# Kernel optimization log

Measured on AMD Instinct MI355X. Metric: run time of the kernel, lower is better.

The kernel has to match this reference:

```python
import jax, jax.numpy as jnp
import numpy as np

N = 1024
C_LOCAL = 384
C_PAIR = 128
HEADS = 8
KEY_SIZE = 32
LN_EPS = 1e-5


def setup_inputs() -> dict:
    key = jax.random.key(0)
    ks = jax.random.split(key, 5)
    local = jax.random.normal(ks[0], (N, C_LOCAL), dtype=jnp.float32)
    pair = jax.random.normal(ks[1], (N, N, C_PAIR), dtype=jnp.float32)
    mask = jnp.ones((N,), dtype=bool)
    ln_scale = jnp.ones((C_LOCAL,), dtype=jnp.float32)
    ln_offset = jnp.zeros((C_LOCAL,), dtype=jnp.float32)
    W_value = jax.random.normal(ks[2], (C_LOCAL, HEADS * KEY_SIZE), dtype=jnp.float32) * (1.0 / np.sqrt(C_LOCAL))
    W_attn = jax.random.normal(ks[3], (C_PAIR, HEADS), dtype=jnp.float32) * (1.0 / np.sqrt(C_PAIR))
    W_out = jax.random.normal(ks[4], (HEADS * KEY_SIZE, C_LOCAL), dtype=jnp.float32) * (1.0 / np.sqrt(HEADS * KEY_SIZE))
    return {"local": local, "pair": pair, "mask": mask,
            "ln_scale": ln_scale, "ln_offset": ln_offset,
            "W_value": W_value, "W_attn": W_attn, "W_out": W_out}


def reference(local, pair, mask, ln_scale, ln_offset, W_value, W_attn, W_out):
    # pair_mask[i, j] = mask[i] & mask[j]
    pair_mask = (mask[:, None] & mask[None, :])[..., None]  # [N, N, 1]

    # LayerNorm over last axis (create_scale=True, create_offset=True)
    mu = jnp.mean(local, axis=-1, keepdims=True)
    var = jnp.var(local, axis=-1, keepdims=True)
    local_ln = (local - mu) * jax.lax.rsqrt(var + LN_EPS) * ln_scale + ln_offset

    # value projection -> [N, heads, key_size]
    value = (local_ln @ W_value).reshape(local.shape[0], HEADS, KEY_SIZE)

    # pair-bias attention logits -> [N, N, heads]
    attn = pair @ W_attn
    attn = jnp.where(pair_mask, attn, -1e9)
    attn = jax.nn.softmax(attn, axis=1)
    attn = jnp.where(pair_mask, attn, 0.0)

    # weighted average over j, per head -> [N, heads, key_size] -> [N, heads*key_size]
    out = jnp.einsum('ijh,jhc->ihc', attn, value).reshape(local.shape[0], -1)
    return out @ W_out
```

## Files before the change

kernel.cpp:

```cpp
#include <hip/hip_runtime.h>
#include <cstddef>

#define NN 1024
#define CL 384
#define CP 128
#define NH 8
#define KS 32
#define HK 256

typedef float floatx4 __attribute__((ext_vector_type(4)));

template<int CTRL>
__device__ __forceinline__ float dpp_mov(float v) {
    return __int_as_float(__builtin_amdgcn_update_dpp(
        0, __float_as_int(v), CTRL, 0xF, 0xF, true));
}

__device__ __forceinline__ float4 ntload4(const float* p) {
    floatx4 t = __builtin_nontemporal_load((const floatx4*)p);
    float4 r; r.x = t.x; r.y = t.y; r.z = t.z; r.w = t.w;
    return r;
}

__global__ __launch_bounds__(256) void k_ln_value(
    const float* __restrict__ local_, const float* __restrict__ ln_scale,
    const float* __restrict__ ln_offset, const float* __restrict__ Wv,
    float* __restrict__ value)
{
    __shared__ float ln_s[4][CL];
    const int tid = threadIdx.x;
    const int w = tid >> 6, lane = tid & 63;
    const int r = blockIdx.x * 4 + w;
    const float* lp = local_ + (size_t)r * CL;
    float x[6]; float s1 = 0.f, s2 = 0.f;
#pragma unroll
    for (int k = 0; k < 6; ++k) { x[k] = lp[lane + 64*k]; s1 += x[k]; s2 += x[k]*x[k]; }
#pragma unroll
    for (int m = 1; m < 64; m <<= 1) { s1 += __shfl_xor(s1, m); s2 += __shfl_xor(s2, m); }
    const float mean = s1 * (1.f/CL);
    const float var  = fmaxf(s2 * (1.f/CL) - mean*mean, 0.f);
    const float rstd = rsqrtf(var + 1e-5f);
#pragma unroll
    for (int k = 0; k < 6; ++k) {
        const int c = lane + 64*k;
        ln_s[w][c] = (x[k]-mean)*rstd*ln_scale[c] + ln_offset[c];
    }
    __syncthreads();
    const int m_ = tid;
    float acc0=0.f, acc1=0.f, acc2=0.f, acc3=0.f;
    for (int c0 = 0; c0 < CL; c0 += 8) {
        float wv[8];
#pragma unroll
        for (int cc = 0; cc < 8; ++cc) wv[cc] = Wv[(size_t)(c0+cc)*HK + m_];
        {
            const float4 a = *(const float4*)&ln_s[0][c0];
            const float4 b = *(const float4*)&ln_s[0][c0+4];
            acc0 += a.x*wv[0]+a.y*wv[1]+a.z*wv[2]+a.w*wv[3]+b.x*wv[4]+b.y*wv[5]+b.z*wv[6]+b.w*wv[7];
        }
        {
            const float4 a = *(const float4*)&ln_s[1][c0];
            const float4 b = *(const float4*)&ln_s[1][c0+4];
            acc1 += a.x*wv[0]+a.y*wv[1]+a.z*wv[2]+a.w*wv[3]+b.x*wv[4]+b.y*wv[5]+b.z*wv[6]+b.w*wv[7];
        }
        {
            const float4 a = *(const float4*)&ln_s[2][c0];
            const float4 b = *(const float4*)&ln_s[2][c0+4];
            acc2 += a.x*wv[0]+a.y*wv[1]+a.z*wv[2]+a.w*wv[3]+b.x*wv[4]+b.y*wv[5]+b.z*wv[6]+b.w*wv[7];
        }
        {
            const float4 a = *(const float4*)&ln_s[3][c0];
            const float4 b = *(const float4*)&ln_s[3][c0+4];
            acc3 += a.x*wv[0]+a.y*wv[1]+a.z*wv[2]+a.w*wv[3]+b.x*wv[4]+b.y*wv[5]+b.z*wv[6]+b.w*wv[7];
        }
    }
    const int rb = blockIdx.x*4;
    value[(size_t)(rb+0)*HK + m_] = acc0;
    value[(size_t)(rb+1)*HK + m_] = acc1;
    value[(size_t)(rb+2)*HK + m_] = acc2;
    value[(size_t)(rb+3)*HK + m_] = acc3;
}

__global__ __launch_bounds__(256, 4) void k_attn(
    const float* __restrict__ pair, const int* __restrict__ mask,
    const float* __restrict__ Wa, const float* __restrict__ value,
    const float* __restrict__ Wo, float* __restrict__ outp)
{
    __shared__ float zf[NN];
    __shared__ float ps[2][NH][68];
    __shared__ float sep[8*NH];
    __shared__ float ov4[4][64][4];
    __shared__ float ov[HK];

    const int tid = threadIdx.x;
    const int g = tid >> 5;
    const int sub5 = tid & 31;
    const int i = blockIdx.x;
    const bool bmi = mask[i] != 0;

    for (int k = tid; k < NN; k += 256)
        zf[k] = (bmi && (mask[k] != 0)) ? 1.f : 0.f;

    float wreg[32];
    {
        const float4* wp = (const float4*)(Wa + sub5*4*NH);
#pragma unroll
        for (int k = 0; k < 8; ++k) {
            const float4 t4 = wp[k];
            wreg[4*k+0]=t4.x; wreg[4*k+1]=t4.y; wreg[4*k+2]=t4.z; wreg[4*k+3]=t4.w;
        }
    }

    const int  myh   = (sub5 & 1)*4 + ((sub5 >> 1) & 1)*2 + ((sub5 >> 3) & 1);
    const bool owner = (sub5 & 0x14) == 0;

    const int q  = tid >> 6;
    const int mq = tid & 63;
    const int pvh = mq >> 3;
    float4 ac4; ac4.x = ac4.y = ac4.z = ac4.w = 0.f;
    float se_loc = 0.f;

    const float* pb = pair + (size_t)i*NN*CP + sub5*4;

    float4 d[8];
#pragma unroll
    for (int s = 0; s < 8; ++s)
        d[s] = ntload4(pb + (size_t)(g*8 + s)*CP);

    __syncthreads();

    for (int ci = 0; ci < 16; ++ci) {
        const int b = ci & 1;
        const int jc = ci * 64;

#pragma unroll
        for (int s = 0; s < 8; ++s) {
            const float4 cur = d[s];
            float acc[8];
#pragma unroll
            for (int h = 0; h < 8; ++h)
                acc[h] = cur.x*wreg[h] + cur.y*wreg[8+h] + cur.z*wreg[16+h] + cur.w*wreg[24+h];
            const bool b0 = (sub5 & 1) != 0;
            const bool b1 = (sub5 & 2) != 0;
            const bool b3 = (sub5 & 8) != 0;
            float r4[4];
#pragma unroll
            for (int k = 0; k < 4; ++k)
                r4[k] = (b0 ? acc[k+4] : acc[k]) + dpp_mov<0xB1>(b0 ? acc[k] : acc[k+4]);
            float r2[2];
#pragma unroll
            for (int k = 0; k < 2; ++k)
                r2[k] = (b1 ? r4[k+2] : r4[k]) + dpp_mov<0x4E>(b1 ? r4[k] : r4[k+2]);
            float r1 = (b3 ? r2[1] : r2[0]) + dpp_mov<0x128>(b3 ? r2[0] : r2[1]);
            r1 += __shfl_xor(r1, 4);
            r1 += __shfl_xor(r1, 16);
            const int jj = g*8 + s;
            const float pt = zf[jc + jj] * __expf(r1);
            se_loc += pt;
            ps[b][myh][jj] = pt;
        }

        if (ci != 15) {
            const int jb = jc + 64 + g*8;
#pragma unroll
            for (int s = 0; s < 8; ++s)
                d[s] = ntload4(pb + (size_t)(jb + s)*CP);
        }

        if (ci > 0) {
            const int pbuf = (ci - 1) & 1;
            const float* vb = value + (size_t)(jc - 64)*HK + mq*4;
#pragma unroll 4
            for (int k = 0; k < 16; ++k) {
                const int jj = 4*k + q;
                const float p = ps[pbuf][pvh][jj];
                const float4 v4 = *(const float4*)(vb + (size_t)jj*HK);
                ac4.x += p*v4.x; ac4.y += p*v4.y; ac4.z += p*v4.z; ac4.w += p*v4.w;
            }
        }

        asm volatile("s_waitcnt lgkmcnt(0)" ::: "memory");
        __builtin_amdgcn_s_barrier();
    }

    {
        const float* vb = value + (size_t)(15*64)*HK + mq*4;
#pragma unroll 4
        for (int k = 0; k < 16; ++k) {
            const int jj = 4*k + q;
            const float p = ps[1][pvh][jj];
            const float4 v4 = *(const float4*)(vb + (size_t)jj*HK);
            ac4.x += p*v4.x; ac4.y += p*v4.y; ac4.z += p*v4.z; ac4.w += p*v4.w;
        }
    }

    if (owner) sep[g*NH + myh] = se_loc;
    ov4[q][mq][0] = ac4.x; ov4[q][mq][1] = ac4.y;
    ov4[q][mq][2] = ac4.z; ov4[q][mq][3] = ac4.w;
    __syncthreads();

    {
        const int m = tid;
        const float s4 = ov4[0][m>>2][m&3] + ov4[1][m>>2][m&3]
                       + ov4[2][m>>2][m&3] + ov4[3][m>>2][m&3];
        const int h = m >> 5;
        float se = 0.f;
#pragma unroll
        for (int k = 0; k < 8; ++k) se += sep[k*NH + h];
        const float inv = (se > 0.f) ? (1.f/se) : 0.f;
        ov[m] = s4 * inv;
    }
    __syncthreads();

    for (int o = tid; o < CL; o += 256) {
        float a0 = 0.f;
        for (int m = 0; m < HK; m += 4) {
            const float4 x0 = *(const float4*)&ov[m];
            a0 += x0.x*Wo[(size_t)(m+0)*CL + o] + x0.y*Wo[(size_t)(m+1)*CL + o]
                + x0.z*Wo[(size_t)(m+2)*CL + o] + x0.w*Wo[(size_t)(m+3)*CL + o];
        }
        outp[(size_t)i*CL + o] = a0;
    }
}

extern "C" void kernel_launch(void* const* d_in, const int* in_sizes, int n_in,
                              void* d_out, int out_size, void* d_ws, size_t ws_size,
                              hipStream_t stream)
{
    (void)in_sizes; (void)n_in; (void)out_size; (void)ws_size;
    const float* local_ = (const float*)d_in[0];
    const float* pair   = (const float*)d_in[1];
    const int*   mask   = (const int*)d_in[2];
    const float* scale  = (const float*)d_in[3];
    const float* offset = (const float*)d_in[4];
    const float* Wv     = (const float*)d_in[5];
    const float* Wa     = (const float*)d_in[6];
    const float* Wo     = (const float*)d_in[7];
    float* value = (float*)d_ws;
    k_ln_value<<<NN/4, 256, 0, stream>>>(local_, scale, offset, Wv, value);
    k_attn<<<NN, 256, 0, stream>>>(pair, mask, Wa, value, Wo, (float*)d_out);
}
```

Before: 149.0 us.

## Restructure attention loop into 32-row chunks with two-deep register prefetch

The pair-logit loop now works on 32-row chunks and keeps two register buffers (dA/dB) of pair data in flight. Each buffer is refilled two chunks ahead, and scheduling barriers keep the prefetch loads from being reordered. The aim is to keep more HBM loads outstanding and hide streaming latency behind the logit and PV compute. The cost is twice as many block barriers, with the same register footprint for the pair data.

```diff
diff --git a/kernel.cpp b/kernel.cpp
--- a/kernel.cpp
+++ b/kernel.cpp
@@ -7,6 +7,8 @@
 #define NH 8
 #define KS 32
 #define HK 256
+#define CHK 32
+#define NCHK (NN/CHK)
 
 typedef float floatx4 __attribute__((ext_vector_type(4)));
 
@@ -86,7 +88,7 @@
     const float* __restrict__ Wo, float* __restrict__ outp)
 {
     __shared__ float zf[NN];
-    __shared__ float ps[2][NH][68];
+    __shared__ float ps[2][NH][CHK+4];
     __shared__ float sep[8*NH];
     __shared__ float ov4[4][64][4];
     __shared__ float ov[HK];
@@ -121,19 +123,17 @@
 
     const float* pb = pair + (size_t)i*NN*CP + sub5*4;
 
-    float4 d[8];
-#pragma unroll
-    for (int s = 0; s < 8; ++s)
-        d[s] = ntload4(pb + (size_t)(g*8 + s)*CP);
-
-    __syncthreads();
-
-    for (int ci = 0; ci < 16; ++ci) {
-        const int b = ci & 1;
-        const int jc = ci * 64;
-
-#pragma unroll
-        for (int s = 0; s < 8; ++s) {
+    float4 dA[4], dB[4];
+
+    auto PREFETCH = [&](float4* d, int jc) {
+#pragma unroll
+        for (int s = 0; s < 4; ++s)
+            d[s] = ntload4(pb + (size_t)(jc + g*4 + s)*CP);
+    };
+
+    auto LOGITS = [&](const float4* d, int jc, int pbuf) {
+#pragma unroll
+        for (int s = 0; s < 4; ++s) {
             const float4 cur = d[s];
             float acc[8];
 #pragma unroll
@@ -153,45 +153,44 @@
             float r1 = (b3 ? r2[1] : r2[0]) + dpp_mov<0x128>(b3 ? r2[0] : r2[1]);
             r1 += __shfl_xor(r1, 4);
             r1 += __shfl_xor(r1, 16);
-            const int jj = g*8 + s;
+            const int jj = g*4 + s;
             const float pt = zf[jc + jj] * __expf(r1);
             se_loc += pt;
-            ps[b][myh][jj] = pt;
-        }
-
-        if (ci != 15) {
-            const int jb = jc + 64 + g*8;
-#pragma unroll
-            for (int s = 0; s < 8; ++s)
-                d[s] = ntload4(pb + (size_t)(jb + s)*CP);
-        }
-
-        if (ci > 0) {
-            const int pbuf = (ci - 1) & 1;
-            const float* vb = value + (size_t)(jc - 64)*HK + mq*4;
-#pragma unroll 4
-            for (int k = 0; k < 16; ++k) {
-                const int jj = 4*k + q;
-                const float p = ps[pbuf][pvh][jj];
-                const float4 v4 = *(const float4*)(vb + (size_t)jj*HK);
-                ac4.x += p*v4.x; ac4.y += p*v4.y; ac4.z += p*v4.z; ac4.w += p*v4.w;
-            }
-        }
-
+            ps[pbuf][myh][jj] = pt;
+        }
+    };
+
+    auto PV = [&](int jc, int pbuf) {
+        const float* vb = value + (size_t)jc*HK + mq*4;
+#pragma unroll
+        for (int k = 0; k < 8; ++k) {
+            const int jj = 4*k + q;
+            const float p = ps[pbuf][pvh][jj];
+            const float4 v4 = *(const float4*)(vb + (size_t)jj*HK);
+            ac4.x += p*v4.x; ac4.y += p*v4.y; ac4.z += p*v4.z; ac4.w += p*v4.w;
+        }
+    };
+
+    PREFETCH(dA, 0);
+    PREFETCH(dB, CHK);
+    __syncthreads();
+
+    for (int it = 0; it < NCHK/2; ++it) {
+        const int k0 = it*2;
+        LOGITS(dA, k0*CHK, 0);
+        if (k0 > 0) PV((k0-1)*CHK, 1);
+        __builtin_amdgcn_sched_barrier(0);
+        if (k0+2 < NCHK) PREFETCH(dA, (k0+2)*CHK);
         asm volatile("s_waitcnt lgkmcnt(0)" ::: "memory");
         __builtin_amdgcn_s_barrier();
-    }
-
-    {
-        const float* vb = value + (size_t)(15*64)*HK + mq*4;
-#pragma unroll 4
-        for (int k = 0; k < 16; ++k) {
-            const int jj = 4*k + q;
-            const float p = ps[1][pvh][jj];
-            const float4 v4 = *(const float4*)(vb + (size_t)jj*HK);
-            ac4.x += p*v4.x; ac4.y += p*v4.y; ac4.z += p*v4.z; ac4.w += p*v4.w;
-        }
-    }
+        LOGITS(dB, (k0+1)*CHK, 1);
+        PV(k0*CHK, 0);
+        __builtin_amdgcn_sched_barrier(0);
+        if (k0+3 < NCHK) PREFETCH(dB, (k0+3)*CHK);
+        asm volatile("s_waitcnt lgkmcnt(0)" ::: "memory");
+        __builtin_amdgcn_s_barrier();
+    }
+    PV((NCHK-1)*CHK, 1);
 
     if (owner) sep[g*NH + myh] = se_loc;
     ov4[q][mq][0] = ac4.x; ov4[q][mq][1] = ac4.y;
```

Measured after the change: 164.5 us. +10.4%, slower.

## Stream pair and value tiles into LDS via async global_load_lds double buffering

Applied to the files above, without the earlier changes.

Replaces the register-held nontemporal prefetch of the pair row with direct global-to-LDS async loads (global_load_lds). The pair row is now processed in 16-row double-buffered tiles, and value rows are staged into LDS per tile as well, with vmcnt waits doing the synchronisation. The aim is to relieve register pressure and overlap memory traffic with compute. In exchange it uses smaller chunks with two barriers per chunk, which means many more iterations and barriers, and occupancy drops to 2 blocks via launch bounds plus a much larger LDS footprint.

```diff
diff --git a/kernel.cpp b/kernel.cpp
--- a/kernel.cpp
+++ b/kernel.cpp
@@ -7,8 +7,8 @@
 #define NH 8
 #define KS 32
 #define HK 256
-
-typedef float floatx4 __attribute__((ext_vector_type(4)));
+#define CKR 16
+#define NB (NN/CKR)
 
 template<int CTRL>
 __device__ __forceinline__ float dpp_mov(float v) {
@@ -16,10 +16,10 @@
         0, __float_as_int(v), CTRL, 0xF, 0xF, true));
 }
 
-__device__ __forceinline__ float4 ntload4(const float* p) {
-    floatx4 t = __builtin_nontemporal_load((const floatx4*)p);
-    float4 r; r.x = t.x; r.y = t.y; r.z = t.z; r.w = t.w;
-    return r;
+__device__ __forceinline__ void glds16(const float* g, float* l) {
+    __builtin_amdgcn_global_load_lds(
+        (const __attribute__((address_space(1))) unsigned int*)g,
+        (__attribute__((address_space(3))) unsigned int*)l, 16, 0, 0);
 }
 
 __global__ __launch_bounds__(256) void k_ln_value(
@@ -80,23 +80,35 @@
     value[(size_t)(rb+3)*HK + m_] = acc3;
 }
 
-__global__ __launch_bounds__(256, 4) void k_attn(
+__global__ __launch_bounds__(256, 2) void k_attn(
     const float* __restrict__ pair, const int* __restrict__ mask,
     const float* __restrict__ Wa, const float* __restrict__ value,
     const float* __restrict__ Wo, float* __restrict__ outp)
 {
+    __shared__ float pairB[2][CKR][CP];
+    __shared__ float valB[CKR][HK];
     __shared__ float zf[NN];
-    __shared__ float ps[2][NH][68];
-    __shared__ float sep[8*NH];
+    __shared__ float ps[NH][CKR+4];
+    __shared__ float sep[8][NH];
     __shared__ float ov4[4][64][4];
     __shared__ float ov[HK];
 
-    const int tid = threadIdx.x;
-    const int g = tid >> 5;
+    const int tid  = threadIdx.x;
+    const int g    = tid >> 5;
     const int sub5 = tid & 31;
     const int i = blockIdx.x;
     const bool bmi = mask[i] != 0;
 
+    const float* prow = pair + (size_t)i*NN*CP;
+
+    {
+        const int r0 = tid >> 5, c0 = (tid & 31) * 4;
+        const float* pg = prow + (size_t)r0*CP + c0;
+        float* lb = &pairB[0][0][0] + tid*4;
+        glds16(pg, lb);
+        glds16(pg + (size_t)8*CP, lb + 1024);
+    }
+
     for (int k = tid; k < NN; k += 256)
         zf[k] = (bmi && (mask[k] != 0)) ? 1.f : 0.f;
 
@@ -116,84 +128,76 @@
     const int q  = tid >> 6;
     const int mq = tid & 63;
     const int pvh = mq >> 3;
+
     float4 ac4; ac4.x = ac4.y = ac4.z = ac4.w = 0.f;
     float se_loc = 0.f;
 
-    const float* pb = pair + (size_t)i*NN*CP + sub5*4;
-
-    float4 d[8];
-#pragma unroll
-    for (int s = 0; s < 8; ++s)
-        d[s] = ntload4(pb + (size_t)(g*8 + s)*CP);
-
-    __syncthreads();
-
-    for (int ci = 0; ci < 16; ++ci) {
-        const int b = ci & 1;
-        const int jc = ci * 64;
-
-#pragma unroll
-        for (int s = 0; s < 8; ++s) {
-            const float4 cur = d[s];
-            float acc[8];
-#pragma unroll
-            for (int h = 0; h < 8; ++h)
-                acc[h] = cur.x*wreg[h] + cur.y*wreg[8+h] + cur.z*wreg[16+h] + cur.w*wreg[24+h];
-            const bool b0 = (sub5 & 1) != 0;
-            const bool b1 = (sub5 & 2) != 0;
-            const bool b3 = (sub5 & 8) != 0;
-            float r4[4];
+    __syncthreads();
+
+    for (int t = 0; t < NB; ++t) {
+        const int j0 = t*CKR;
+        {
+            const int r = tid >> 6, c = (tid & 63)*4;
+            const float* vg = value + (size_t)(j0 + r)*HK + c;
+            float* lb = &valB[0][0] + tid*4;
 #pragma unroll
             for (int k = 0; k < 4; ++k)
-                r4[k] = (b0 ? acc[k+4] : acc[k]) + dpp_mov<0xB1>(b0 ? acc[k] : acc[k+4]);
-            float r2[2];
-#pragma unroll
-            for (int k = 0; k < 2; ++k)
-                r2[k] = (b1 ? r4[k+2] : r4[k]) + dpp_mov<0x4E>(b1 ? r4[k] : r4[k+2]);
-            float r1 = (b3 ? r2[1] : r2[0]) + dpp_mov<0x128>(b3 ? r2[0] : r2[1]);
-            r1 += __shfl_xor(r1, 4);
-            r1 += __shfl_xor(r1, 16);
-            const int jj = g*8 + s;
-            const float pt = zf[jc + jj] * __expf(r1);
-            se_loc += pt;
-            ps[b][myh][jj] = pt;
-        }
-
-        if (ci != 15) {
-            const int jb = jc + 64 + g*8;
-#pragma unroll
-            for (int s = 0; s < 8; ++s)
-                d[s] = ntload4(pb + (size_t)(jb + s)*CP);
-        }
-
-        if (ci > 0) {
-            const int pbuf = (ci - 1) & 1;
-            const float* vb = value + (size_t)(jc - 64)*HK + mq*4;
-#pragma unroll 4
-            for (int k = 0; k < 16; ++k) {
-                const int jj = 4*k + q;
-                const float p = ps[pbuf][pvh][jj];
-                const float4 v4 = *(const float4*)(vb + (size_t)jj*HK);
+                glds16(vg + (size_t)(k*4)*HK, lb + k*1024);
+        }
+        const bool more = (t+1 < NB);
+        if (more) {
+            const int r0 = tid >> 5, c0 = (tid & 31)*4;
+            const float* pg = prow + (size_t)((t+1)*CKR + r0)*CP + c0;
+            float* lb = &pairB[(t+1)&1][0][0] + tid*4;
+            glds16(pg, lb);
+            glds16(pg + (size_t)8*CP, lb + 1024);
+        }
+        {
+            const float* pbuf = &pairB[t&1][0][0];
+#pragma unroll
+            for (int s = 0; s < 2; ++s) {
+                const int row = g*2 + s;
+                const float4 c = *(const float4*)(pbuf + row*CP + sub5*4);
+                float acc[8];
+#pragma unroll
+                for (int h = 0; h < 8; ++h)
+                    acc[h] = c.x*wreg[h] + c.y*wreg[8+h] + c.z*wreg[16+h] + c.w*wreg[24+h];
+                const bool b0 = (sub5 & 1) != 0;
+                const bool b1 = (sub5 & 2) != 0;
+                const bool b3 = (sub5 & 8) != 0;
+                float r4[4];
+#pragma unroll
+                for (int k = 0; k < 4; ++k)
+                    r4[k] = (b0 ? acc[k+4] : acc[k]) + dpp_mov<0xB1>(b0 ? acc[k] : acc[k+4]);
+                float r2[2];
+#pragma unroll
+                for (int k = 0; k < 2; ++k)
+                    r2[k] = (b1 ? r4[k+2] : r4[k]) + dpp_mov<0x4E>(b1 ? r4[k] : r4[k+2]);
+                float r1 = (b3 ? r2[1] : r2[0]) + dpp_mov<0x128>(b3 ? r2[0] : r2[1]);
+                r1 += __shfl_xor(r1, 4);
+                r1 += __shfl_xor(r1, 16);
+                const float pt = zf[j0 + row] * __expf(r1);
+                se_loc += pt;
+                ps[myh][row] = pt;
+            }
+        }
+        if (more) asm volatile("s_waitcnt vmcnt(2) lgkmcnt(0)" ::: "memory");
+        else      asm volatile("s_waitcnt vmcnt(0) lgkmcnt(0)" ::: "memory");
+        __builtin_amdgcn_s_barrier();
+        {
+#pragma unroll
+            for (int k = 0; k < 4; ++k) {
+                const int j = k*4 + q;
+                const float p = ps[pvh][j];
+                const float4 v4 = *(const float4*)(&valB[j][mq*4]);
                 ac4.x += p*v4.x; ac4.y += p*v4.y; ac4.z += p*v4.z; ac4.w += p*v4.w;
             }
         }
-
-        asm volatile("s_waitcnt lgkmcnt(0)" ::: "memory");
+        asm volatile("s_waitcnt vmcnt(0) lgkmcnt(0)" ::: "memory");
         __builtin_amdgcn_s_barrier();
     }
 
-    {
-        const float* vb = value + (size_t)(15*64)*HK + mq*4;
-#pragma unroll 4
-        for (int k = 0; k < 16; ++k) {
-            const int jj = 4*k + q;
-            const float p = ps[1][pvh][jj];
-            const float4 v4 = *(const float4*)(vb + (size_t)jj*HK);
-            ac4.x += p*v4.x; ac4.y += p*v4.y; ac4.z += p*v4.z; ac4.w += p*v4.w;
-        }
-    }
-
-    if (owner) sep[g*NH + myh] = se_loc;
+    if (owner) sep[g][myh] = se_loc;
     ov4[q][mq][0] = ac4.x; ov4[q][mq][1] = ac4.y;
     ov4[q][mq][2] = ac4.z; ov4[q][mq][3] = ac4.w;
     __syncthreads();
@@ -205,7 +209,7 @@
         const int h = m >> 5;
         float se = 0.f;
 #pragma unroll
-        for (int k = 0; k < 8; ++k) se += sep[k*NH + h];
+        for (int k = 0; k < 8; ++k) se += sep[k][h];
         const float inv = (se > 0.f) ? (1.f/se) : 0.f;
         ov[m] = s4 * inv;
     }
```

Result: slower. 234.1 us (+57.2%).
